# Optimization experiments

Measured on AMD Instinct MI355X. Metric: run time of the kernel, lower is better.

The kernel has to match this reference:

```python
import jax, jax.numpy as jnp
import numpy as np

HID = 1024       # hidden_size
H = 8            # num_attention_heads
KVH = 2          # num_key_value_heads
D = HID // H     # head_dim = 128
WINDOW = 2048    # sliding_window
THETA = 10000.0  # rope_theta
B, S = 1, 4096


def rotate_half(x):
    x1, x2 = jnp.split(x, 2, axis=-1)
    return jnp.concatenate([-x2, x1], axis=-1)


def setup_inputs() -> dict:
    key = jax.random.key(0)
    ks = jax.random.split(key, 5)
    scale = 0.02
    return {
        "hidden_states": jax.random.normal(ks[0], (B, S, HID), dtype=jnp.float32),
        "wq": jax.random.normal(ks[1], (H * D, HID), dtype=jnp.float32) * scale,
        "wk": jax.random.normal(ks[2], (KVH * D, HID), dtype=jnp.float32) * scale,
        "wv": jax.random.normal(ks[3], (KVH * D, HID), dtype=jnp.float32) * scale,
        "wo": jax.random.normal(ks[4], (HID, H * D), dtype=jnp.float32) * scale,
        "position_ids": jnp.broadcast_to(jnp.arange(S, dtype=jnp.int64 if jax.config.jax_enable_x64 else jnp.int32)[None, :], (B, S)),
    }


def reference(hidden_states, wq, wk, wv, wo, position_ids):
    b, s, _ = hidden_states.shape
    # projections (torch nn.Linear: x @ W^T)
    q = (hidden_states @ wq.T).reshape(b, s, H, D).transpose(0, 2, 1, 3)      # bhsd
    k = (hidden_states @ wk.T).reshape(b, s, KVH, D).transpose(0, 2, 1, 3)    # b(kv)sd
    v = (hidden_states @ wv.T).reshape(b, s, KVH, D).transpose(0, 2, 1, 3)

    # RoPE cache (head_dim, seq_len)
    inv_freq = 1.0 / THETA ** (jnp.arange(0, D, 2, dtype=jnp.float32) / D)
    t = jnp.arange(s, dtype=jnp.float32)
    freqs = t[:, None] * inv_freq[None, :]
    emb = jnp.concatenate([freqs, freqs], axis=-1)           # (S, D)
    cos = jnp.cos(emb)[position_ids][:, None]                # (B,1,S,D)
    sin = jnp.sin(emb)[position_ids][:, None]
    q = q * cos + rotate_half(q) * sin
    k = k * cos + rotate_half(k) * sin

    # GQA: repeat kv heads to match query heads (repeat_interleave on head dim)
    groups = H // KVH
    k = jnp.repeat(k, groups, axis=1)
    v = jnp.repeat(v, groups, axis=1)

    # full score matrix with sliding-window causal mask
    scores = jnp.einsum("bhqd,bhkd->bhqk", q, k)
    i = jnp.arange(s)[:, None]
    j = jnp.arange(s)[None, :]
    mask = (j <= i) & (j > i - WINDOW)                       # causal + window
    scores = jnp.where(mask[None, None], scores, -jnp.inf) / jnp.sqrt(jnp.float32(D))

    probs = jax.nn.softmax(scores.astype(jnp.float32), axis=-1).astype(q.dtype)
    ctx = jnp.einsum("bhqk,bhkd->bhqd", probs, v)
    ctx = ctx.transpose(0, 2, 1, 3).reshape(b, s, H * D)
    return ctx @ wo.T
```

## Files before the change

kernel.cpp:

```cpp
#include <hip/hip_runtime.h>

#define S_LEN 4096
#define HIDDEN 1024
#define NH 8
#define NKV 2
#define HD 128
#define WIN 2048

typedef short bf16x8 __attribute__((ext_vector_type(8)));
typedef float f32x4 __attribute__((ext_vector_type(4)));
typedef unsigned short u16x4 __attribute__((ext_vector_type(4)));

__device__ __forceinline__ unsigned short f2b(float f) {
    unsigned int u = __builtin_bit_cast(unsigned int, f);
    u += 0x7fffu + ((u >> 16) & 1u);
    return (unsigned short)(u >> 16);
}
__device__ __forceinline__ float b2f(unsigned short u) {
    unsigned int x = ((unsigned int)u) << 16;
    return __builtin_bit_cast(float, x);
}

__device__ __forceinline__ void gl_lds16(const unsigned short* g, unsigned short* l) {
    __builtin_amdgcn_global_load_lds(
        (const __attribute__((address_space(1))) unsigned int*)g,
        (__attribute__((address_space(3))) unsigned int*)l, 16, 0, 0);
}

#define WAIT_VM4   0x0F74
#define WAIT_VM0   0x0F70
#define WAIT_LGKM0 0xC07F
#define MEMFENCE() __asm__ volatile("" ::: "memory")

__global__ __launch_bounds__(256) void cvt5(
    const float* __restrict__ s0, unsigned short* __restrict__ t0, int n0,
    const float* __restrict__ s1, unsigned short* __restrict__ t1, int n1,
    const float* __restrict__ s2, unsigned short* __restrict__ t2, int n2,
    const float* __restrict__ s3, unsigned short* __restrict__ t3, int n3,
    const float* __restrict__ s4, unsigned short* __restrict__ t4, int n4)
{
    int i = blockIdx.x * 256 + threadIdx.x;
    const float* s; unsigned short* t;
    if (i < n0)              { s = s0; t = t0; }
    else if ((i -= n0) < n1) { s = s1; t = t1; }
    else if ((i -= n1) < n2) { s = s2; t = t2; }
    else if ((i -= n2) < n3) { s = s3; t = t3; }
    else if ((i -= n3) < n4) { s = s4; t = t4; }
    else return;
    f32x4 v = *(const f32x4*)(s + (size_t)i * 4);
    u16x4 r = { f2b(v[0]), f2b(v[1]), f2b(v[2]), f2b(v[3]) };
    *(u16x4*)(t + (size_t)i * 4) = r;
}

__global__ __launch_bounds__(256, 2) void gemm128(
    const unsigned short* __restrict__ A, const unsigned short* __restrict__ W,
    float* __restrict__ Cf, unsigned short* __restrict__ Cb,
    int M, int N, int K)
{
    __shared__ alignas(16) unsigned short As[2][128 * 32];
    __shared__ alignas(16) unsigned short Bs[2][128 * 32];

    int lane = threadIdx.x & 63;
    int w = threadIdx.x >> 6;
    int l15 = lane & 15, quad = lane >> 4;

    int tiles_n = N >> 7;
    int mt0 = (int)blockIdx.x / tiles_n;
    int nt0 = (int)blockIdx.x - mt0 * tiles_n;

    size_t goffA[2], goffB[2];
    #pragma unroll
    for (int is = 0; is < 2; ++is) {
        int s = w * 128 + is * 64 + lane;
        int row = s >> 2, spos = s & 3;
        int kblk = spos ^ ((row >> 1) & 3);
        goffA[is] = (size_t)(mt0 * 128 + row) * K + kblk * 8;
        goffB[is] = (size_t)(nt0 * 128 + row) * K + kblk * 8;
    }

    int arow0 = (w >> 1) * 64;
    int brow0 = (w & 1) * 64;
    int aoff[4], boff[4];
    #pragma unroll
    for (int t = 0; t < 4; ++t) {
        int ra = arow0 + t * 16 + l15;
        aoff[t] = (ra * 4 + (quad ^ ((ra >> 1) & 3))) * 8;
        int rb = brow0 + t * 16 + l15;
        boff[t] = (rb * 4 + (quad ^ ((rb >> 1) & 3))) * 8;
    }

    f32x4 acc[4][4];
    #pragma unroll
    for (int i = 0; i < 4; ++i)
        #pragma unroll
        for (int j = 0; j < 4; ++j) acc[i][j] = (f32x4){0.f, 0.f, 0.f, 0.f};

    auto stage = [&](int i) {
        int b = i & 1, k0 = i * 32;
        gl_lds16(A + goffA[0] + k0, &As[b][(w * 128 + 0) * 8]);
        gl_lds16(A + goffA[1] + k0, &As[b][(w * 128 + 64) * 8]);
        gl_lds16(W + goffB[0] + k0, &Bs[b][(w * 128 + 0) * 8]);
        gl_lds16(W + goffB[1] + k0, &Bs[b][(w * 128 + 64) * 8]);
    };

    int nk = K >> 5;
    stage(0);
    for (int i = 0; i < nk; ++i) {
        if (i + 1 < nk) {
            stage(i + 1);
            MEMFENCE();
            __builtin_amdgcn_s_waitcnt(WAIT_VM4);
        } else {
            MEMFENCE();
            __builtin_amdgcn_s_waitcnt(WAIT_VM0);
        }
        __builtin_amdgcn_s_barrier();
        MEMFENCE();

        const unsigned short* Ab = &As[i & 1][0];
        const unsigned short* Bb = &Bs[i & 1][0];
        bf16x8 af[4], bf_[4];
        #pragma unroll
        for (int t = 0; t < 4; ++t) {
            af[t]  = *(const bf16x8*)(Ab + aoff[t]);
            bf_[t] = *(const bf16x8*)(Bb + boff[t]);
        }
        #pragma unroll
        for (int i2 = 0; i2 < 4; ++i2)
            #pragma unroll
            for (int j = 0; j < 4; ++j)
                acc[i2][j] = __builtin_amdgcn_mfma_f32_16x16x32_bf16(af[i2], bf_[j], acc[i2][j], 0, 0, 0);

        MEMFENCE();
        __builtin_amdgcn_s_waitcnt(WAIT_LGKM0);
        __builtin_amdgcn_s_barrier();
        MEMFENCE();
    }

    #pragma unroll
    for (int i = 0; i < 4; ++i) {
        int row0 = mt0 * 128 + arow0 + i * 16 + quad * 4;
        #pragma unroll
        for (int j = 0; j < 4; ++j) {
            int col = nt0 * 128 + brow0 + j * 16 + l15;
            if (Cf) {
                #pragma unroll
                for (int reg = 0; reg < 4; ++reg)
                    Cf[(size_t)(row0 + reg) * N + col] = acc[i][j][reg];
            } else {
                #pragma unroll
                for (int reg = 0; reg < 4; ++reg)
                    Cb[(size_t)(row0 + reg) * N + col] = f2b(acc[i][j][reg]);
            }
        }
    }
}

#define QKVW (HIDDEN + 2 * NKV * HD)
__global__ __launch_bounds__(256, 2) void gemmqkv(
    const unsigned short* __restrict__ A, const unsigned short* __restrict__ W,
    const int* __restrict__ pos,
    unsigned short* __restrict__ Qb, unsigned short* __restrict__ Kb,
    unsigned short* __restrict__ Vg)
{
    __shared__ alignas(16) unsigned short As[2][128 * 32];
    __shared__ alignas(16) unsigned short Bs[2][128 * 32];
    __shared__ float Ex[4][32][68];

    int lane = threadIdx.x & 63;
    int w = threadIdx.x >> 6;
    int l15 = lane & 15, quad = lane >> 4;

    const int K = HIDDEN;
    int mt0 = (int)blockIdx.x / 12;
    int nt0 = (int)blockIdx.x - mt0 * 12;

    size_t goffA[2], goffB[2];
    #pragma unroll
    for (int is = 0; is < 2; ++is) {
        int s = w * 128 + is * 64 + lane;
        int row = s >> 2, spos = s & 3;
        int kblk = spos ^ ((row >> 1) & 3);
        goffA[is] = (size_t)(mt0 * 128 + row) * K + kblk * 8;
        goffB[is] = (size_t)(nt0 * 128 + row) * K + kblk * 8;
    }

    int arow0 = (w >> 1) * 64;
    int brow0 = (w & 1) * 64;
    int aoff[4], boff[4];
    #pragma unroll
    for (int t = 0; t < 4; ++t) {
        int ra = arow0 + t * 16 + l15;
        aoff[t] = (ra * 4 + (quad ^ ((ra >> 1) & 3))) * 8;
        int rb = brow0 + t * 16 + l15;
        boff[t] = (rb * 4 + (quad ^ ((rb >> 1) & 3))) * 8;
    }

    f32x4 acc[4][4];
    #pragma unroll
    for (int i = 0; i < 4; ++i)
        #pragma unroll
        for (int j = 0; j < 4; ++j) acc[i][j] = (f32x4){0.f, 0.f, 0.f, 0.f};

    auto stage = [&](int i) {
        int b = i & 1, k0 = i * 32;
        gl_lds16(A + goffA[0] + k0, &As[b][(w * 128 + 0) * 8]);
        gl_lds16(A + goffA[1] + k0, &As[b][(w * 128 + 64) * 8]);
        gl_lds16(W + goffB[0] + k0, &Bs[b][(w * 128 + 0) * 8]);
        gl_lds16(W + goffB[1] + k0, &Bs[b][(w * 128 + 64) * 8]);
    };

    stage(0);
    for (int i = 0; i < 32; ++i) {
        if (i + 1 < 32) {
            stage(i + 1);
            MEMFENCE();
            __builtin_amdgcn_s_waitcnt(WAIT_VM4);
        } else {
            MEMFENCE();
            __builtin_amdgcn_s_waitcnt(WAIT_VM0);
        }
        __builtin_amdgcn_s_barrier();
        MEMFENCE();

        const unsigned short* Ab = &As[i & 1][0];
        const unsigned short* Bb = &Bs[i & 1][0];
        bf16x8 af[4], bf_[4];
        #pragma unroll
        for (int t = 0; t < 4; ++t) {
            af[t]  = *(const bf16x8*)(Ab + aoff[t]);
            bf_[t] = *(const bf16x8*)(Bb + boff[t]);
        }
        #pragma unroll
        for (int i2 = 0; i2 < 4; ++i2)
            #pragma unroll
            for (int j = 0; j < 4; ++j)
                acc[i2][j] = __builtin_amdgcn_mfma_f32_16x16x32_bf16(af[i2], bf_[j], acc[i2][j], 0, 0, 0);

        MEMFENCE();
        __builtin_amdgcn_s_waitcnt(WAIT_LGKM0);
        __builtin_amdgcn_s_barrier();
        MEMFENCE();
    }

    if (nt0 >= 10) {
        int kv = nt0 - 10;
        #pragma unroll
        for (int i = 0; i < 4; ++i) {
            int row0 = mt0 * 128 + arow0 + i * 16 + quad * 4;
            #pragma unroll
            for (int j = 0; j < 4; ++j) {
                int col = kv * 128 + brow0 + j * 16 + l15;
                #pragma unroll
                for (int reg = 0; reg < 4; ++reg)
                    Vg[(size_t)(row0 + reg) * (NKV * HD) + col] = f2b(acc[i][j][reg]);
            }
        }
        return;
    }

    bool isQ = (nt0 < 8);
    int kv = nt0 - 8;
    bool is64 = (pos[1] == 0) && (pos[3] == 0);
    const float qscale = 0.08838834764831843f;

    float invf[4];
    #pragma unroll
    for (int j = 0; j < 4; ++j) {
        int d6 = (brow0 + j * 16 + l15) & 63;
        invf[j] = exp2f(-(float)d6 * (13.287712379549449f / 64.0f));
    }

    #pragma unroll
    for (int r2 = 0; r2 < 2; ++r2) {
        #pragma unroll
        for (int ii = 0; ii < 2; ++ii) {
            int i = r2 * 2 + ii;
            #pragma unroll
            for (int j = 0; j < 4; ++j)
                #pragma unroll
                for (int reg = 0; reg < 4; ++reg)
                    Ex[w][ii * 16 + quad * 4 + reg][j * 16 + l15] = acc[i][j][reg];
        }
        __syncthreads();
        #pragma unroll
        for (int ii = 0; ii < 2; ++ii) {
            int i = r2 * 2 + ii;
            #pragma unroll
            for (int reg = 0; reg < 4; ++reg) {
                int s = mt0 * 128 + arow0 + i * 16 + quad * 4 + reg;
                int pv_ = is64 ? pos[2 * s] : pos[s];
                float pf = (float)pv_;
                #pragma unroll
                for (int j = 0; j < 4; ++j) {
                    float sn, cs;
                    __sincosf(pf * invf[j], &sn, &cs);
                    float a  = acc[i][j][reg];
                    float pr = Ex[w ^ 1][ii * 16 + quad * 4 + reg][j * 16 + l15];
                    int d_local = brow0 + j * 16 + l15;
                    float outv = (d_local < 64) ? (a * cs - pr * sn) : (a * cs + pr * sn);
                    if (isQ) {
                        Qb[(size_t)s * HIDDEN + nt0 * HD + d_local] = f2b(outv * qscale);
                    } else {
                        Kb[(size_t)kv * S_LEN * HD + (size_t)s * HD + d_local] = f2b(outv);
                    }
                }
            }
        }
        __syncthreads();
    }
}

__global__ __launch_bounds__(256) void vtrans(
    const unsigned short* __restrict__ Vg, unsigned short* __restrict__ Vt)
{
    __shared__ unsigned short L[64][66];
    int st = (int)blockIdx.x >> 2, dt = (int)blockIdx.x & 3;
    int s0 = st * 64, d0 = dt * 64;
    int tid = threadIdx.x;
    {
        int dl = tid & 63, sl4 = tid >> 6;
        #pragma unroll
        for (int p = 0; p < 16; ++p) {
            int sl = p * 4 + sl4;
            L[sl][dl] = Vg[(size_t)(s0 + sl) * (NKV * HD) + d0 + dl];
        }
    }
    __syncthreads();
    {
        int sl = tid & 63, dl4 = tid >> 6;
        #pragma unroll
        for (int p = 0; p < 16; ++p) {
            int dl = p * 4 + dl4;
            Vt[(size_t)(d0 + dl) * S_LEN + s0 + sl] = L[sl][dl];
        }
    }
}

__global__ __launch_bounds__(256, 4) void attn_coop(
    const unsigned short* __restrict__ Qb, const unsigned short* __restrict__ Kb,
    const unsigned short* __restrict__ Vt, unsigned short* __restrict__ Ctx)
{
    __shared__ alignas(16) unsigned short Klds[2][32 * 128];
    __shared__ alignas(16) unsigned short Vlds[2][128 * 32];
    __shared__ alignas(16) unsigned short Plds[4][512];

    int lane = threadIdx.x & 63;
    int w = threadIdx.x >> 6;
    int l15 = lane & 15, quad = lane >> 4;
    int h = blockIdx.y;
    int kv = h >> 2;
    int qb = blockIdx.x * 64;
    int q16 = qb + w * 16;

    bf16x8 a_q[4];
    const unsigned short* qrow = Qb + (size_t)(q16 + l15) * HIDDEN + h * HD + quad * 8;
    #pragma unroll
    for (int st = 0; st < 4; ++st) a_q[st] = *(const bf16x8*)(qrow + st * 32);

    bf16x8 b_one;
    #pragma unroll
    for (int i = 0; i < 8; ++i) b_one[i] = (short)0x3F80;

    int lo = qb + 63 - (WIN - 1); if (lo < 0) lo = 0; lo &= ~31;
    int nch = (qb + 64 - lo) >> 5;

    const unsigned short* kbaseG = Kb + (size_t)kv * S_LEN * HD;
    const unsigned short* vbaseG = Vt + (size_t)kv * HD * S_LEN;
    int offK[2], dstK[2], offV[2], dstV[2];
    #pragma unroll
    for (int tt = 0; tt < 2; ++tt) {
        int t = w * 2 + tt;
        int key  = t * 4 + (lane >> 4);
        int dblk = (lane & 15) ^ (key & 15);
        offK[tt] = key * HD + dblk * 8;
        dstK[tt] = t * 512;
        int d    = t * 16 + (lane >> 2);
        int kblk = (lane & 3) ^ (d & 3);
        offV[tt] = d * S_LEN + kblk * 8;
        dstV[tt] = t * 512;
    }

    auto issue = [&](int c) {
        int j0 = lo + c * 32;
        int b = c & 1;
        const unsigned short* ks = kbaseG + (size_t)j0 * HD;
        const unsigned short* vs = vbaseG + j0;
        gl_lds16(ks + offK[0], &Klds[b][dstK[0]]);
        gl_lds16(ks + offK[1], &Klds[b][dstK[1]]);
        gl_lds16(vs + offV[0], &Vlds[b][dstV[0]]);
        gl_lds16(vs + offV[1], &Vlds[b][dstV[1]]);
    };

    f32x4 o[9];
    #pragma unroll
    for (int nd = 0; nd < 9; ++nd) o[nd] = (f32x4){0.f, 0.f, 0.f, 0.f};

    unsigned short* pw = &Plds[w][0];

    int pwr[2][4];
    #pragma unroll
    for (int t = 0; t < 2; ++t)
        #pragma unroll
        for (int reg = 0; reg < 4; ++reg) {
            int row = quad * 4 + reg;
            int slot = row * 4 + (((t * 2) + (l15 >> 3)) ^ (row & 3));
            pwr[t][reg] = slot * 8 + (l15 & 7);
        }
    int prd = (l15 * 4 + (quad ^ (l15 & 3))) * 8;

    issue(0);

    for (int c = 0; c < nch; ++c) {
        int j0 = lo + c * 32;
        if (c + 1 < nch) {
            issue(c + 1);
            MEMFENCE();
            __builtin_amdgcn_s_waitcnt(WAIT_VM4);
        } else {
            MEMFENCE();
            __builtin_amdgcn_s_waitcnt(WAIT_VM0);
        }
        __builtin_amdgcn_s_barrier();
        MEMFENCE();

        const unsigned short* Kc = &Klds[c & 1][0];
        const unsigned short* Vc = &Vlds[c & 1][0];

        f32x4 sc[2];
        #pragma unroll
        for (int t = 0; t < 2; ++t) {
            sc[t] = (f32x4){0.f, 0.f, 0.f, 0.f};
            int key = t * 16 + l15;
            #pragma unroll
            for (int st = 0; st < 4; ++st) {
                int off16 = key * 16 + ((st * 4 + quad) ^ (key & 15));
                bf16x8 bk = *(const bf16x8*)(Kc + off16 * 8);
                sc[t] = __builtin_amdgcn_mfma_f32_16x16x32_bf16(a_q[st], bk, sc[t], 0, 0, 0);
            }
        }

        float p[2][4];
        if (j0 + 31 <= q16 && j0 > q16 + 15 - WIN) {
            #pragma unroll
            for (int t = 0; t < 2; ++t)
                #pragma unroll
                for (int reg = 0; reg < 4; ++reg) p[t][reg] = __expf(sc[t][reg]);
        } else {
            #pragma unroll
            for (int t = 0; t < 2; ++t) {
                int jj = j0 + t * 16 + l15;
                #pragma unroll
                for (int reg = 0; reg < 4; ++reg) {
                    int i = q16 + quad * 4 + reg;
                    p[t][reg] = (jj <= i && jj > i - WIN) ? __expf(sc[t][reg]) : 0.f;
                }
            }
        }

        #pragma unroll
        for (int t = 0; t < 2; ++t)
            #pragma unroll
            for (int reg = 0; reg < 4; ++reg)
                pw[pwr[t][reg]] = f2b(p[t][reg]);

        __builtin_amdgcn_wave_barrier();
        __builtin_amdgcn_s_waitcnt(WAIT_LGKM0);
        __builtin_amdgcn_wave_barrier();

        bf16x8 a_p = *(const bf16x8*)(pw + prd);

        #pragma unroll
        for (int nd = 0; nd < 8; ++nd) {
            int d = nd * 16 + l15;
            int o16 = d * 4 + (quad ^ (d & 3));
            bf16x8 bv = *(const bf16x8*)(Vc + o16 * 8);
            o[nd] = __builtin_amdgcn_mfma_f32_16x16x32_bf16(a_p, bv, o[nd], 0, 0, 0);
        }
        o[8] = __builtin_amdgcn_mfma_f32_16x16x32_bf16(a_p, b_one, o[8], 0, 0, 0);

        MEMFENCE();
        __builtin_amdgcn_s_waitcnt(WAIT_LGKM0);
        __builtin_amdgcn_s_barrier();
        MEMFENCE();
    }

    #pragma unroll
    for (int nd = 0; nd < 8; ++nd) {
        int d = nd * 16 + l15;
        #pragma unroll
        for (int reg = 0; reg < 4; ++reg) {
            int q = q16 + quad * 4 + reg;
            Ctx[(size_t)q * HIDDEN + h * HD + d] = f2b(o[nd][reg] / o[8][reg]);
        }
    }
}

extern "C" void kernel_launch(void* const* d_in, const int* in_sizes, int n_in,
                              void* d_out, int out_size, void* d_ws, size_t ws_size,
                              hipStream_t stream)
{
    const float* hidden = (const float*)d_in[0];
    const float* wq = (const float*)d_in[1];
    const float* wk = (const float*)d_in[2];
    const float* wv = (const float*)d_in[3];
    const float* wo = (const float*)d_in[4];
    const int* pos = (const int*)d_in[5];
    float* out = (float*)d_out;

    char* ws = (char*)d_ws;
    size_t off = 0;
    unsigned short* Hb   = (unsigned short*)(ws + off); off += (size_t)S_LEN * HIDDEN * 2;
    unsigned short* Wqkv = (unsigned short*)(ws + off); off += (size_t)QKVW * HIDDEN * 2;
    unsigned short* Wob  = (unsigned short*)(ws + off); off += (size_t)HIDDEN * HIDDEN * 2;
    unsigned short* Qb   = (unsigned short*)(ws + off); off += (size_t)S_LEN * HIDDEN * 2;
    unsigned short* Kb   = (unsigned short*)(ws + off); off += (size_t)S_LEN * NKV * HD * 2;
    unsigned short* Vg   = (unsigned short*)(ws + off); off += (size_t)S_LEN * NKV * HD * 2;
    unsigned short* Vt   = (unsigned short*)(ws + off); off += (size_t)S_LEN * NKV * HD * 2;
    unsigned short* Cb   = (unsigned short*)(ws + off); off += (size_t)S_LEN * HIDDEN * 2;

    const int n_h  = S_LEN * HIDDEN / 4;
    const int n_wq = HIDDEN * HIDDEN / 4;
    const int n_wk = NKV * HD * HIDDEN / 4;
    int tot4 = n_h + n_wq + 2 * n_wk + n_wq;
    cvt5<<<(tot4 + 255) / 256, 256, 0, stream>>>(
        hidden, Hb, n_h,
        wq, Wqkv, n_wq,
        wk, Wqkv + (size_t)HIDDEN * HIDDEN, n_wk,
        wv, Wqkv + (size_t)(HIDDEN + NKV * HD) * HIDDEN, n_wk,
        wo, Wob, n_wq);

    gemmqkv<<<(S_LEN / 128) * 12, 256, 0, stream>>>(
        Hb, Wqkv, pos, Qb, Kb, Vg);

    vtrans<<<(S_LEN / 64) * ((NKV * HD) / 64), 256, 0, stream>>>(Vg, Vt);

    attn_coop<<<dim3(S_LEN / 64, NH), 256, 0, stream>>>(Qb, Kb, Vt, Cb);

    gemm128<<<(S_LEN / 128) * (HIDDEN / 128), 256, 0, stream>>>(
        Cb, Wob, out, nullptr, S_LEN, HIDDEN, HIDDEN);
}
```

Baseline: 209.9 us.

## Fuse V transpose into QKV GEMM and restructure attention to 64-key chunks

```diff
diff --git a/kernel.cpp b/kernel.cpp
--- a/kernel.cpp
+++ b/kernel.cpp
@@ -8,6 +8,7 @@
 #define WIN 2048
 
 typedef short bf16x8 __attribute__((ext_vector_type(8)));
+typedef short bf16x4 __attribute__((ext_vector_type(4)));
 typedef float f32x4 __attribute__((ext_vector_type(4)));
 typedef unsigned short u16x4 __attribute__((ext_vector_type(4)));
 
@@ -27,6 +28,7 @@
         (__attribute__((address_space(3))) unsigned int*)l, 16, 0, 0);
 }
 
+#define WAIT_VM8   0x0F78
 #define WAIT_VM4   0x0F74
 #define WAIT_VM0   0x0F70
 #define WAIT_LGKM0 0xC07F
@@ -161,7 +163,7 @@
     const unsigned short* __restrict__ A, const unsigned short* __restrict__ W,
     const int* __restrict__ pos,
     unsigned short* __restrict__ Qb, unsigned short* __restrict__ Kb,
-    unsigned short* __restrict__ Vg)
+    unsigned short* __restrict__ Vt)
 {
     __shared__ alignas(16) unsigned short As[2][128 * 32];
     __shared__ alignas(16) unsigned short Bs[2][128 * 32];
@@ -245,16 +247,29 @@
 
     if (nt0 >= 10) {
         int kv = nt0 - 10;
+        unsigned short* T = (unsigned short*)&Ex[0][0][0];
         #pragma unroll
         for (int i = 0; i < 4; ++i) {
-            int row0 = mt0 * 128 + arow0 + i * 16 + quad * 4;
+            int srow = arow0 + i * 16 + quad * 4;
             #pragma unroll
             for (int j = 0; j < 4; ++j) {
-                int col = kv * 128 + brow0 + j * 16 + l15;
+                int d = brow0 + j * 16 + l15;
                 #pragma unroll
                 for (int reg = 0; reg < 4; ++reg)
-                    Vg[(size_t)(row0 + reg) * (NKV * HD) + col] = f2b(acc[i][j][reg]);
+                    T[(srow + reg) * 130 + d] = f2b(acc[i][j][reg]);
             }
+        }
+        __syncthreads();
+        int tid = threadIdx.x;
+        int dl = tid >> 5;
+        int sc4 = (tid & 31) * 4;
+        #pragma unroll
+        for (int it = 0; it < 16; ++it) {
+            int d = it * 8 + dl;
+            u16x4 v4 = { T[(sc4 + 0) * 130 + d], T[(sc4 + 1) * 130 + d],
+                         T[(sc4 + 2) * 130 + d], T[(sc4 + 3) * 130 + d] };
+            *(u16x4*)(Vt + (size_t)kv * HD * S_LEN + (size_t)d * S_LEN
+                      + mt0 * 128 + sc4) = v4;
         }
         return;
     }
@@ -311,39 +326,12 @@
     }
 }
 
-__global__ __launch_bounds__(256) void vtrans(
-    const unsigned short* __restrict__ Vg, unsigned short* __restrict__ Vt)
-{
-    __shared__ unsigned short L[64][66];
-    int st = (int)blockIdx.x >> 2, dt = (int)blockIdx.x & 3;
-    int s0 = st * 64, d0 = dt * 64;
-    int tid = threadIdx.x;
-    {
-        int dl = tid & 63, sl4 = tid >> 6;
-        #pragma unroll
-        for (int p = 0; p < 16; ++p) {
-            int sl = p * 4 + sl4;
-            L[sl][dl] = Vg[(size_t)(s0 + sl) * (NKV * HD) + d0 + dl];
-        }
-    }
-    __syncthreads();
-    {
-        int sl = tid & 63, dl4 = tid >> 6;
-        #pragma unroll
-        for (int p = 0; p < 16; ++p) {
-            int dl = p * 4 + dl4;
-            Vt[(size_t)(d0 + dl) * S_LEN + s0 + sl] = L[sl][dl];
-        }
-    }
-}
-
-__global__ __launch_bounds__(256, 4) void attn_coop(
+__global__ __launch_bounds__(256, 2) void attn_coop(
     const unsigned short* __restrict__ Qb, const unsigned short* __restrict__ Kb,
     const unsigned short* __restrict__ Vt, unsigned short* __restrict__ Ctx)
 {
-    __shared__ alignas(16) unsigned short Klds[2][32 * 128];
-    __shared__ alignas(16) unsigned short Vlds[2][128 * 32];
-    __shared__ alignas(16) unsigned short Plds[4][512];
+    __shared__ alignas(16) unsigned short Klds[2][64 * 128];
+    __shared__ alignas(16) unsigned short Vlds[2][128 * 64];
 
     int lane = threadIdx.x & 63;
     int w = threadIdx.x >> 6;
@@ -358,65 +346,64 @@
     #pragma unroll
     for (int st = 0; st < 4; ++st) a_q[st] = *(const bf16x8*)(qrow + st * 32);
 
-    bf16x8 b_one;
-    #pragma unroll
-    for (int i = 0; i < 8; ++i) b_one[i] = (short)0x3F80;
-
-    int lo = qb + 63 - (WIN - 1); if (lo < 0) lo = 0; lo &= ~31;
-    int nch = (qb + 64 - lo) >> 5;
-
-    const unsigned short* kbaseG = Kb + (size_t)kv * S_LEN * HD;
-    const unsigned short* vbaseG = Vt + (size_t)kv * HD * S_LEN;
-    int offK[2], dstK[2], offV[2], dstV[2];
-    #pragma unroll
-    for (int tt = 0; tt < 2; ++tt) {
-        int t = w * 2 + tt;
-        int key  = t * 4 + (lane >> 4);
-        int dblk = (lane & 15) ^ (key & 15);
-        offK[tt] = key * HD + dblk * 8;
-        dstK[tt] = t * 512;
-        int d    = t * 16 + (lane >> 2);
-        int kblk = (lane & 3) ^ (d & 3);
-        offV[tt] = d * S_LEN + kblk * 8;
-        dstV[tt] = t * 512;
+    bf16x4 ones4;
+    #pragma unroll
+    for (int i = 0; i < 4; ++i) ones4[i] = (short)0x3F80;
+
+    int lo = qb + 63 - (WIN - 1); if (lo < 0) lo = 0; lo &= ~63;
+    int nch = (qb + 64 - lo) >> 6;
+
+    const unsigned short* gbase;
+    unsigned short* ldsdst[2];
+    int myoff[8];
+    int jmul;
+    if (w < 2) {
+        gbase = Kb + (size_t)kv * S_LEN * HD;
+        ldsdst[0] = &Klds[0][w * 8 * 512];
+        ldsdst[1] = &Klds[1][w * 8 * 512];
+        jmul = HD;
+        #pragma unroll
+        for (int tt = 0; tt < 8; ++tt) {
+            int t = w * 8 + tt;
+            int key  = t * 4 + (lane >> 4);
+            int dblk = (lane & 15) ^ (key & 15);
+            myoff[tt] = key * HD + dblk * 8;
+        }
+    } else {
+        gbase = Vt + (size_t)kv * HD * S_LEN;
+        ldsdst[0] = &Vlds[0][(w - 2) * 8 * 512];
+        ldsdst[1] = &Vlds[1][(w - 2) * 8 * 512];
+        jmul = 1;
+        #pragma unroll
+        for (int tt = 0; tt < 8; ++tt) {
+            int t = (w - 2) * 8 + tt;
+            int d    = t * 8 + (lane >> 3);
+            int kblk = (lane & 7) ^ (d & 7);
+            myoff[tt] = d * S_LEN + kblk * 8;
+        }
     }
 
     auto issue = [&](int c) {
-        int j0 = lo + c * 32;
-        int b = c & 1;
-        const unsigned short* ks = kbaseG + (size_t)j0 * HD;
-        const unsigned short* vs = vbaseG + j0;
-        gl_lds16(ks + offK[0], &Klds[b][dstK[0]]);
-        gl_lds16(ks + offK[1], &Klds[b][dstK[1]]);
-        gl_lds16(vs + offV[0], &Vlds[b][dstV[0]]);
-        gl_lds16(vs + offV[1], &Vlds[b][dstV[1]]);
+        int j0 = lo + c * 64;
+        const unsigned short* src = gbase + (size_t)j0 * jmul;
+        unsigned short* dst = ldsdst[c & 1];
+        #pragma unroll
+        for (int tt = 0; tt < 8; ++tt)
+            gl_lds16(src + myoff[tt], dst + tt * 512);
     };
 
     f32x4 o[9];
     #pragma unroll
     for (int nd = 0; nd < 9; ++nd) o[nd] = (f32x4){0.f, 0.f, 0.f, 0.f};
 
-    unsigned short* pw = &Plds[w][0];
-
-    int pwr[2][4];
-    #pragma unroll
-    for (int t = 0; t < 2; ++t)
-        #pragma unroll
-        for (int reg = 0; reg < 4; ++reg) {
-            int row = quad * 4 + reg;
-            int slot = row * 4 + (((t * 2) + (l15 >> 3)) ^ (row & 3));
-            pwr[t][reg] = slot * 8 + (l15 & 7);
-        }
-    int prd = (l15 * 4 + (quad ^ (l15 & 3))) * 8;
-
     issue(0);
 
     for (int c = 0; c < nch; ++c) {
-        int j0 = lo + c * 32;
+        int j0 = lo + c * 64;
         if (c + 1 < nch) {
             issue(c + 1);
             MEMFENCE();
-            __builtin_amdgcn_s_waitcnt(WAIT_VM4);
+            __builtin_amdgcn_s_waitcnt(WAIT_VM8);
         } else {
             MEMFENCE();
             __builtin_amdgcn_s_waitcnt(WAIT_VM0);
@@ -427,57 +414,58 @@
         const unsigned short* Kc = &Klds[c & 1][0];
         const unsigned short* Vc = &Vlds[c & 1][0];
 
-        f32x4 sc[2];
-        #pragma unroll
-        for (int t = 0; t < 2; ++t) {
+        f32x4 sc[4];
+        #pragma unroll
+        for (int t = 0; t < 4; ++t) {
             sc[t] = (f32x4){0.f, 0.f, 0.f, 0.f};
             int key = t * 16 + l15;
             #pragma unroll
             for (int st = 0; st < 4; ++st) {
                 int off16 = key * 16 + ((st * 4 + quad) ^ (key & 15));
-                bf16x8 bk = *(const bf16x8*)(Kc + off16 * 8);
-                sc[t] = __builtin_amdgcn_mfma_f32_16x16x32_bf16(a_q[st], bk, sc[t], 0, 0, 0);
+                bf16x8 ak = *(const bf16x8*)(Kc + off16 * 8);
+                sc[t] = __builtin_amdgcn_mfma_f32_16x16x32_bf16(ak, a_q[st], sc[t], 0, 0, 0);
             }
         }
 
-        float p[2][4];
-        if (j0 + 31 <= q16 && j0 > q16 + 15 - WIN) {
-            #pragma unroll
-            for (int t = 0; t < 2; ++t)
+        float p[4][4];
+        if (j0 + 63 <= q16 && j0 > q16 + 15 - WIN) {
+            #pragma unroll
+            for (int t = 0; t < 4; ++t)
                 #pragma unroll
                 for (int reg = 0; reg < 4; ++reg) p[t][reg] = __expf(sc[t][reg]);
         } else {
-            #pragma unroll
-            for (int t = 0; t < 2; ++t) {
-                int jj = j0 + t * 16 + l15;
+            int iq = q16 + l15;
+            #pragma unroll
+            for (int t = 0; t < 4; ++t) {
                 #pragma unroll
                 for (int reg = 0; reg < 4; ++reg) {
-                    int i = q16 + quad * 4 + reg;
-                    p[t][reg] = (jj <= i && jj > i - WIN) ? __expf(sc[t][reg]) : 0.f;
+                    int key = j0 + t * 16 + quad * 4 + reg;
+                    p[t][reg] = (key <= iq && key > iq - WIN) ? __expf(sc[t][reg]) : 0.f;
                 }
             }
         }
 
-        #pragma unroll
-        for (int t = 0; t < 2; ++t)
-            #pragma unroll
-            for (int reg = 0; reg < 4; ++reg)
-                pw[pwr[t][reg]] = f2b(p[t][reg]);
-
-        __builtin_amdgcn_wave_barrier();
-        __builtin_amdgcn_s_waitcnt(WAIT_LGKM0);
-        __builtin_amdgcn_wave_barrier();
-
-        bf16x8 a_p = *(const bf16x8*)(pw + prd);
-
-        #pragma unroll
-        for (int nd = 0; nd < 8; ++nd) {
-            int d = nd * 16 + l15;
-            int o16 = d * 4 + (quad ^ (d & 3));
-            bf16x8 bv = *(const bf16x8*)(Vc + o16 * 8);
-            o[nd] = __builtin_amdgcn_mfma_f32_16x16x32_bf16(a_p, bv, o[nd], 0, 0, 0);
-        }
-        o[8] = __builtin_amdgcn_mfma_f32_16x16x32_bf16(a_p, b_one, o[8], 0, 0, 0);
+        bf16x4 a_p[4];
+        #pragma unroll
+        for (int t = 0; t < 4; ++t) {
+            a_p[t][0] = (short)f2b(p[t][0]);
+            a_p[t][1] = (short)f2b(p[t][1]);
+            a_p[t][2] = (short)f2b(p[t][2]);
+            a_p[t][3] = (short)f2b(p[t][3]);
+        }
+
+        #pragma unroll
+        for (int t = 0; t < 4; ++t) {
+            #pragma unroll
+            for (int nd = 0; nd < 8; ++nd) {
+                int d = nd * 16 + l15;
+                int kblk = t * 2 + (quad >> 1);
+                int slot = d * 8 + (kblk ^ (d & 7));
+                bf16x4 bv = *(const bf16x4*)(Vc + slot * 8 + (quad & 1) * 4);
+                o[nd] = __builtin_amdgcn_mfma_f32_16x16x16bf16_1k(a_p[t], bv, o[nd], 0, 0, 0);
+            }
+            o[8] = __builtin_amdgcn_mfma_f32_16x16x16bf16_1k(a_p[t], ones4, o[8], 0, 0, 0);
+        }
 
         MEMFENCE();
         __builtin_amdgcn_s_waitcnt(WAIT_LGKM0);
@@ -515,7 +503,6 @@
     unsigned short* Wob  = (unsigned short*)(ws + off); off += (size_t)HIDDEN * HIDDEN * 2;
     unsigned short* Qb   = (unsigned short*)(ws + off); off += (size_t)S_LEN * HIDDEN * 2;
     unsigned short* Kb   = (unsigned short*)(ws + off); off += (size_t)S_LEN * NKV * HD * 2;
-    unsigned short* Vg   = (unsigned short*)(ws + off); off += (size_t)S_LEN * NKV * HD * 2;
     unsigned short* Vt   = (unsigned short*)(ws + off); off += (size_t)S_LEN * NKV * HD * 2;
     unsigned short* Cb   = (unsigned short*)(ws + off); off += (size_t)S_LEN * HIDDEN * 2;
 
@@ -531,9 +518,7 @@
         wo, Wob, n_wq);
 
     gemmqkv<<<(S_LEN / 128) * 12, 256, 0, stream>>>(
-        Hb, Wqkv, pos, Qb, Kb, Vg);
-
-    vtrans<<<(S_LEN / 64) * ((NKV * HD) / 64), 256, 0, stream>>>(Vg, Vt);
+        Hb, Wqkv, pos, Qb, Kb, Vt);
 
     attn_coop<<<dim3(S_LEN / 64, NH), 256, 0, stream>>>(Qb, Kb, Vt, Cb);
 
```

Result: faster. 197.3 us (-6.0%).
